# Performance work log

Hardware: AMD Instinct MI355X
Metric: run time of the kernel (lower is better)

The kernel has to match this reference:

```python
import jax, jax.numpy as jnp
import numpy as np

B = 16      # number of point clouds
N = 4096    # points per cloud (max after densify)
D = 3       # xyz


def setup_inputs() -> dict:
    key = jax.random.key(0)
    k1, k2 = jax.random.split(key)
    pred = jax.random.normal(k1, (B * N, D), dtype=jnp.float32)
    target = jax.random.normal(k2, (B * N, D), dtype=jnp.float32)
    # sorted segment ids, equal-sized clouds (faithful to to_dense_batch usage)
    batch = jnp.repeat(jnp.arange(B, dtype=jnp.int64), N)
    return {"pred": pred, "target": target, "batch": batch}


def to_dense_batch(x, batch, num_batches, max_n):
    # PyG to_dense_batch: scatter flat points into [B, max_n, D], zero-padded.
    ones = jnp.ones_like(batch)
    counts = jax.ops.segment_sum(ones, batch, num_segments=num_batches)
    offsets = jnp.concatenate([jnp.zeros((1,), batch.dtype), jnp.cumsum(counts)[:-1]])
    pos = jnp.arange(batch.shape[0], dtype=batch.dtype) - offsets[batch]
    dense = jnp.zeros((num_batches, max_n, x.shape[-1]), x.dtype)
    return dense.at[batch, pos].set(x)


def chamfer_distance(x, y):
    # squared-euclidean pairwise distances via the GEMM identity
    x2 = jnp.sum(x * x, axis=-1)                      # [B, N]
    y2 = jnp.sum(y * y, axis=-1)                      # [B, M]
    xy = jnp.einsum('bnd,bmd->bnm', x, y)             # [B, N, M]
    d = x2[:, :, None] + y2[:, None, :] - 2.0 * xy    # [B, N, M]
    cham_x = jnp.mean(jnp.min(d, axis=2), axis=1)     # mean over N of min over M
    cham_y = jnp.mean(jnp.min(d, axis=1), axis=1)     # mean over M of min over N
    # point_reduction='mean', batch_reduction='mean' (pytorch3d defaults)
    return jnp.mean(cham_x + cham_y)


def reference(pred, target, batch):
    x = to_dense_batch(pred, batch, B, N)
    y = to_dense_batch(target, batch, B, N)
    return chamfer_distance(x, y)
```

## Files before the change

### kernel.cpp

```cpp
#include <hip/hip_runtime.h>


namespace {

constexpr int kB = 16;
constexpr int kN = 4096;
constexpr int kNTH = 256;
constexpr int kTILE = 256;
constexpr int kPlane = kB * kN;
constexpr float kScale = 1.0f / (float)(kB * kN);

__global__ void init_out(float* out) { out[0] = 0.0f; }

template <int KX, int S, bool DIRECT>
__global__ __launch_bounds__(kNTH) void chamfer_min(
    const float* __restrict__ pred, const float* __restrict__ targ,
    float* __restrict__ part, float* __restrict__ out) {
  __shared__ float4 ytile[kTILE];

  const int t = threadIdx.x;
  const int xb = blockIdx.x;
  const int b = blockIdx.y;
  const int z = blockIdx.z;
  const int dir = z / S;
  const int slice = z % S;

  const float* __restrict__ X = dir ? targ : pred;
  const float* __restrict__ Y = dir ? pred : targ;

  float xpx[KX], xpy[KX], xpz[KX], x2[KX], mn[KX];
  const int ibase = b * kN + xb * (kNTH * KX) + t;
#pragma unroll
  for (int k = 0; k < KX; ++k) {
    const int i = ibase + k * kNTH;
    const float a = X[3 * i], c = X[3 * i + 1], d = X[3 * i + 2];
    x2[k] = fmaf(a, a, fmaf(c, c, d * d));
    xpx[k] = -2.0f * a; xpy[k] = -2.0f * c; xpz[k] = -2.0f * d;
    mn[k] = 1e30f;
  }

  constexpr int YSL = kN / S;
  const int ybase = b * kN + slice * YSL;
  for (int t0 = 0; t0 < YSL; t0 += kTILE) {
    const int j = ybase + t0 + t;
    const float a = Y[3 * j], c = Y[3 * j + 1], d = Y[3 * j + 2];
    __syncthreads();
    ytile[t] = make_float4(a, c, d, fmaf(a, a, fmaf(c, c, d * d)));
    __syncthreads();
#pragma unroll 4
    for (int jj = 0; jj < kTILE; jj += 2) {
      const float4 q0 = ytile[jj];
      const float4 q1 = ytile[jj + 1];
#pragma unroll
      for (int k = 0; k < KX; ++k) {
        const float v0 =
            fmaf(xpx[k], q0.x, fmaf(xpy[k], q0.y, fmaf(xpz[k], q0.z, q0.w)));
        const float v1 =
            fmaf(xpx[k], q1.x, fmaf(xpy[k], q1.y, fmaf(xpz[k], q1.z, q1.w)));
        mn[k] = fminf(mn[k], fminf(v0, v1));
      }
    }
  }

  if constexpr (DIRECT) {
    float s = 0.0f;
#pragma unroll
    for (int k = 0; k < KX; ++k) s += x2[k] + mn[k];
    for (int o = 32; o > 0; o >>= 1) s += __shfl_down(s, o, 64);
    __shared__ float wsum[kNTH / 64];
    const int lane = t & 63, w = t >> 6;
    if (lane == 0) wsum[w] = s;
    __syncthreads();
    if (t == 0) {
      float tot = 0.0f;
#pragma unroll
      for (int w2 = 0; w2 < kNTH / 64; ++w2) tot += wsum[w2];
      atomicAdd(out, tot * kScale);
    }
  } else {
#pragma unroll
    for (int k = 0; k < KX; ++k)
      part[(size_t)z * kPlane + (ibase + k * kNTH)] = x2[k] + mn[k];
  }
}

template <int S>
__global__ __launch_bounds__(256) void chamfer_reduce(
    const float* __restrict__ part, float* __restrict__ out) {
  const int u = blockIdx.x * 256 + threadIdx.x;
  const int dir = u >> 16;
  const int q = u & (kPlane - 1);
  float m = 1e30f;
#pragma unroll
  for (int s = 0; s < S; ++s)
    m = fminf(m, part[(size_t)(dir * S + s) * kPlane + q]);
  for (int o = 32; o > 0; o >>= 1) m += __shfl_down(m, o, 64);
  __shared__ float wsum[4];
  const int lane = threadIdx.x & 63, w = threadIdx.x >> 6;
  if (lane == 0) wsum[w] = m;
  __syncthreads();
  if (threadIdx.x == 0)
    atomicAdd(out, (wsum[0] + wsum[1] + wsum[2] + wsum[3]) * kScale);
}

}

extern "C" void kernel_launch(void* const* d_in, const int* in_sizes, int n_in,
                              void* d_out, int out_size, void* d_ws,
                              size_t ws_size, hipStream_t stream) {
  const float* pred = (const float*)d_in[0];
  const float* targ = (const float*)d_in[1];
  float* out = (float*)d_out;
  float* part = (float*)d_ws;

  init_out<<<dim3(1), dim3(1), 0, stream>>>(out);

  constexpr int KX = 4;
  const size_t need8 = (size_t)2 * 8 * kPlane * sizeof(float);
  const size_t need4 = (size_t)2 * 4 * kPlane * sizeof(float);
  if (ws_size >= need8) {
    constexpr int S = 8;
    dim3 grid(kN / (kNTH * KX), kB, 2 * S);
    chamfer_min<KX, S, false><<<grid, kNTH, 0, stream>>>(pred, targ, part, out);
    chamfer_reduce<S><<<dim3(2 * kPlane / 256), 256, 0, stream>>>(part, out);
  } else if (ws_size >= need4) {
    constexpr int S = 4;
    dim3 grid(kN / (kNTH * KX), kB, 2 * S);
    chamfer_min<KX, S, false><<<grid, kNTH, 0, stream>>>(pred, targ, part, out);
    chamfer_reduce<S><<<dim3(2 * kPlane / 256), 256, 0, stream>>>(part, out);
  } else {
    constexpr int KX2 = 2;
    dim3 grid(kN / (kNTH * KX2), kB, 2);
    chamfer_min<KX2, 1, true><<<grid, kNTH, 0, stream>>>(pred, targ, nullptr,
                                                         out);
  }
}
```

Before: 107.4 us.

## Fold output init into min kernel, raise KX and slices, batch reduce per thread

Removes the separate init kernel launch by having every block of the min kernel zero the output before the reduce kernel accumulates into it. The points per thread go from 4 to 8, and a 16-slice split of Y is added when the workspace allows it, which keeps the grid size while doubling register reuse of each y tile. The reduce kernel now handles 8 points per thread, so it launches fewer blocks and issues fewer atomics. Risks are higher register pressure in the min kernel and a larger partial buffer to write and read.

```diff
diff --git a/kernel.cpp b/kernel.cpp
--- a/kernel.cpp
+++ b/kernel.cpp
@@ -24,6 +24,10 @@
   const int z = blockIdx.z;
   const int dir = z / S;
   const int slice = z % S;
+
+  if constexpr (!DIRECT) {
+    if (t == 0) out[0] = 0.0f;
+  }
 
   const float* __restrict__ X = dir ? targ : pred;
   const float* __restrict__ Y = dir ? pred : targ;
@@ -84,20 +88,25 @@
   }
 }
 
-template <int S>
+template <int S, int RQ>
 __global__ __launch_bounds__(256) void chamfer_reduce(
     const float* __restrict__ part, float* __restrict__ out) {
-  const int u = blockIdx.x * 256 + threadIdx.x;
-  const int dir = u >> 16;
-  const int q = u & (kPlane - 1);
-  float m = 1e30f;
+  float s = 0.0f;
 #pragma unroll
-  for (int s = 0; s < S; ++s)
-    m = fminf(m, part[(size_t)(dir * S + s) * kPlane + q]);
-  for (int o = 32; o > 0; o >>= 1) m += __shfl_down(m, o, 64);
+  for (int r = 0; r < RQ; ++r) {
+    const int u = blockIdx.x * (256 * RQ) + r * 256 + threadIdx.x;
+    const int dir = u >> 16;
+    const int q = u & (kPlane - 1);
+    float m = 1e30f;
+#pragma unroll
+    for (int sl = 0; sl < S; ++sl)
+      m = fminf(m, part[(size_t)(dir * S + sl) * kPlane + q]);
+    s += m;
+  }
+  for (int o = 32; o > 0; o >>= 1) s += __shfl_down(s, o, 64);
   __shared__ float wsum[4];
   const int lane = threadIdx.x & 63, w = threadIdx.x >> 6;
-  if (lane == 0) wsum[w] = m;
+  if (lane == 0) wsum[w] = s;
   __syncthreads();
   if (threadIdx.x == 0)
     atomicAdd(out, (wsum[0] + wsum[1] + wsum[2] + wsum[3]) * kScale);
@@ -113,22 +122,31 @@
   float* out = (float*)d_out;
   float* part = (float*)d_ws;
 
-  init_out<<<dim3(1), dim3(1), 0, stream>>>(out);
-
-  constexpr int KX = 4;
+  constexpr int KX = 8;
+  constexpr int RQ = 8;
+  const size_t need16 = (size_t)2 * 16 * kPlane * sizeof(float);
   const size_t need8 = (size_t)2 * 8 * kPlane * sizeof(float);
   const size_t need4 = (size_t)2 * 4 * kPlane * sizeof(float);
-  if (ws_size >= need8) {
+  if (ws_size >= need16) {
+    constexpr int S = 16;
+    dim3 grid(kN / (kNTH * KX), kB, 2 * S);
+    chamfer_min<KX, S, false><<<grid, kNTH, 0, stream>>>(pred, targ, part, out);
+    chamfer_reduce<S, RQ>
+        <<<dim3(2 * kPlane / (256 * RQ)), 256, 0, stream>>>(part, out);
+  } else if (ws_size >= need8) {
     constexpr int S = 8;
     dim3 grid(kN / (kNTH * KX), kB, 2 * S);
     chamfer_min<KX, S, false><<<grid, kNTH, 0, stream>>>(pred, targ, part, out);
-    chamfer_reduce<S><<<dim3(2 * kPlane / 256), 256, 0, stream>>>(part, out);
+    chamfer_reduce<S, RQ>
+        <<<dim3(2 * kPlane / (256 * RQ)), 256, 0, stream>>>(part, out);
   } else if (ws_size >= need4) {
     constexpr int S = 4;
     dim3 grid(kN / (kNTH * KX), kB, 2 * S);
     chamfer_min<KX, S, false><<<grid, kNTH, 0, stream>>>(pred, targ, part, out);
-    chamfer_reduce<S><<<dim3(2 * kPlane / 256), 256, 0, stream>>>(part, out);
+    chamfer_reduce<S, RQ>
+        <<<dim3(2 * kPlane / (256 * RQ)), 256, 0, stream>>>(part, out);
   } else {
+    init_out<<<dim3(1), dim3(1), 0, stream>>>(out);
     constexpr int KX2 = 2;
     dim3 grid(kN / (kNTH * KX2), kB, 2);
     chamfer_min<KX2, 1, true><<<grid, kNTH, 0, stream>>>(pred, targ, nullptr,
```

After: 115.0 us. 7.2% more time.
